# Optimization experiments

Hardware: AMD Instinct MI355X
Metric: run time of the kernel (lower is better)

The kernel has to match this reference:

```python
import jax, jax.numpy as jnp
import numpy as np

NITER = 3

def fft2c(x):
    x = jnp.fft.ifftshift(x, axes=(-2, -1))
    x = jnp.fft.fft2(x, axes=(-2, -1), norm='ortho')
    return jnp.fft.fftshift(x, axes=(-2, -1))

def ifft2c(x):
    x = jnp.fft.ifftshift(x, axes=(-2, -1))
    x = jnp.fft.ifft2(x, axes=(-2, -1), norm='ortho')
    return jnp.fft.fftshift(x, axes=(-2, -1))

def conv3d(x, w):
    # x: [N, D, H, W, C]; w: [3,3,3,Cin,Cout]; 'same' padding, stride 1, no bias
    return jax.lax.conv_general_dilated(x, w, window_strides=(1, 1, 1), padding='SAME',
                                        dimension_numbers=('NDHWC', 'DHWIO', 'NDHWC'))

def setup_inputs():
    key = jax.random.key(0)
    ks = jax.random.split(key, 16)
    nb, nt, nx, ny = 1, 18, 160, 160
    s = 0.05  # weight scale to keep unrolled iterations numerically tame
    d_real = jax.random.normal(ks[0], (nb, nt, nx, ny), jnp.float32)
    d_imag = jax.random.normal(ks[1], (nb, nt, nx, ny), jnp.float32)
    mask = jax.random.randint(ks[2], (nt, nx, ny), 0, 2, jnp.int32)
    W1 = jax.random.normal(ks[3], (NITER, 3, 3, 3, 2, 16), jnp.float32) * s
    W2 = jax.random.normal(ks[4], (NITER, 3, 3, 3, 16, 16), jnp.float32) * s
    W3 = jax.random.normal(ks[5], (NITER, 3, 3, 3, 16, 16), jnp.float32) * s
    W4 = jax.random.normal(ks[6], (NITER, 3, 3, 3, 16, 16), jnp.float32) * s
    W5 = jax.random.normal(ks[7], (NITER, 3, 3, 3, 16, 16), jnp.float32) * s
    W6 = jax.random.normal(ks[8], (NITER, 3, 3, 3, 16, 2), jnp.float32) * s
    lam1 = jnp.full((NITER,), 0.1, jnp.float32)       # lambda_step init
    lam2 = jnp.full((NITER,), 0.1, jnp.float32)       # lambda_step_2 init
    soft_thr = jnp.full((NITER,), 0.1, jnp.float32)
    thres_coef = jnp.full((NITER,), -2.0, jnp.float32)
    eta = jnp.full((NITER,), 0.01, jnp.float32)
    return dict(d_real=d_real, d_imag=d_imag, mask=mask, W1=W1, W2=W2, W3=W3, W4=W4,
                W5=W5, W6=W6, lam1=lam1, lam2=lam2, soft_thr=soft_thr,
                thres_coef=thres_coef, eta=eta)

def _slr_net(d_real, d_imag, mask, W1, W2, W3, W4, W5, W6, lam1, lam2, soft_thr, thres_coef, eta):
    d = jax.lax.complex(d_real, d_imag)          # [nb,nt,nx,ny] complex64
    m = mask.astype(jnp.complex64)               # [nt,nx,ny], broadcasts over batch
    x_rec = ifft2c(d * m)                        # E^H d
    t = jnp.zeros_like(x_rec)
    beta = jnp.zeros_like(x_rec)
    X_SYM = []
    for i in range(NITER):
        lam = jnp.maximum(lam1[i], 0.0).astype(jnp.complex64)
        lam2c = jnp.maximum(lam2[i], 0.0).astype(jnp.complex64)
        # data-consistency gradient: E^H (E x - d)
        ATAX = ifft2c(m * (m * fft2c(x_rec) - d))
        r_n = x_rec - lam * ATAX + lam2c * (x_rec + beta - t)
        r = jnp.stack([r_n.real, r_n.imag], axis=-1)  # [nb,nt,nx,ny,2]
        x1 = jax.nn.relu(conv3d(r, W1[i]))
        x2 = jax.nn.relu(conv3d(x1, W2[i]))
        x3 = conv3d(x2, W3[i])
        x_soft = jnp.sign(x3) * jax.nn.relu(jnp.abs(x3) - soft_thr[i])
        x4 = jax.nn.relu(conv3d(x_soft, W4[i]))
        x5 = jax.nn.relu(conv3d(x4, W5[i]))
        x6 = conv3d(x5, W6[i])
        x_out = x6 + r
        xs = jax.nn.relu(conv3d(x3, W4[i]))
        xs = jax.nn.relu(conv3d(xs, W5[i]))
        xs = conv3d(xs, W6[i])
        x_sym = xs - r
        x_rec = jax.lax.complex(x_out[..., 0], x_out[..., 1])
        # low-rank step: batched thin SVD with learned singular-value thresholding
        nb_, nt_, nx_, ny_ = x_rec.shape
        M = x_rec.reshape(nb_, nt_, nx_ * ny_)
        U, S, Vh = jnp.linalg.svd(M, full_matrices=False)   # U:[b,nt,nt] S:[b,nt] Vh:[b,nt,nx*ny]
        thres = jax.nn.sigmoid(thres_coef[i]) * S[:, :1]
        S = jax.nn.relu(S - thres)
        t = (U * S[:, None, :].astype(U.dtype)) @ Vh
        t = t.reshape(nb_, nt_, nx_, ny_)
        beta = beta + jnp.maximum(eta[i], 0.0).astype(jnp.complex64) * (x_rec - t)
        X_SYM.append(x_sym)
    return x_rec, jnp.stack(X_SYM)

def reference(d_real, d_imag, mask, W1, W2, W3, W4, W5, W6, lam1, lam2, soft_thr, thres_coef, eta):
    return _slr_net(d_real, d_imag, mask, W1, W2, W3, W4, W5, W6, lam1, lam2, soft_thr, thres_coef, eta)
```

## Files before the change

### kernel.cpp

```cpp
#include <hip/hip_runtime.h>
#include <hip/hip_fp16.h>

#define NT 18
#define NX 160
#define NY 160
#define NPIX (NX*NY)
#define NVOX (NT*NPIX)

typedef _Float16 __attribute__((ext_vector_type(2))) half2t;
typedef _Float16 __attribute__((ext_vector_type(8))) half8t;
typedef float    __attribute__((ext_vector_type(4))) f32x4;
typedef unsigned int u32;
typedef __attribute__((address_space(1))) const u32 gu32;
typedef __attribute__((address_space(3))) u32 lu32;

__global__ void probe_kernel(float* __restrict__ out, int n, float val) {
  int i = blockIdx.x * 256 + threadIdx.x;
  if (i < n) out[i] = val;
}

__global__ void make_g_kernel(float2* __restrict__ G) {
  int idx = blockIdx.x * 256 + threadIdx.x;
  if (idx >= NPIX) return;
  int r = idx / NY, c = idx - (idx / NY) * NY;
  int rs = (r + 80) % 160;
  int cs = (c + 80) % 160;
  int prod = (rs * cs) % 160;
  double ang = -2.0 * 3.14159265358979323846 * (double)prod / 160.0;
  double sc = 0.07905694150420949;
  G[idx] = make_float2((float)(cos(ang) * sc), (float)(sin(ang) * sc));
}

__global__ void zero_kernel(float* __restrict__ p, int n) {
  int i = blockIdx.x * 256 + threadIdx.x;
  if (i < n) p[i] = 0.f;
}

template <int MASKD>
__global__ void fft_pass_last4(const float2* __restrict__ in, float2* __restrict__ out,
                               const float2* __restrict__ G, int conjf,
                               const float* __restrict__ dr, const float* __restrict__ di,
                               const int* __restrict__ maskp) {
  __shared__ float2 rows[4][NY];
  int r0 = blockIdx.x * 4;
  int v = threadIdx.x;
#pragma unroll
  for (int r = 0; r < 4; ++r) {
    size_t idx = (size_t)(r0 + r) * NY + v;
    if (MASKD) {
      float m = (float)maskp[idx];
      rows[r][v] = make_float2(m * dr[idx], m * di[idx]);
    } else {
      rows[r][v] = in[idx];
    }
  }
  __syncthreads();
  float sgn = conjf ? -1.f : 1.f;
  float ar[4] = {0.f, 0.f, 0.f, 0.f}, ai[4] = {0.f, 0.f, 0.f, 0.f};
  for (int k = 0; k < NY; ++k) {
    float2 g = G[k * NY + v];
    float gi = sgn * g.y;
#pragma unroll
    for (int r = 0; r < 4; ++r) {
      float2 a = rows[r][k];
      ar[r] += a.x * g.x - a.y * gi;
      ai[r] += a.x * gi + a.y * g.x;
    }
  }
#pragma unroll
  for (int r = 0; r < 4; ++r)
    out[(size_t)(r0 + r) * NY + v] = make_float2(ar[r], ai[r]);
}

template <int EPI>
__global__ void fft_pass_mid4(const float2* __restrict__ in, void* __restrict__ outv,
                              const float2* __restrict__ G, int conjf,
                              const float* __restrict__ dr, const float* __restrict__ di,
                              const int* __restrict__ maskp,
                              const float2* __restrict__ xrec2, const float2* __restrict__ beta2,
                              const float2* __restrict__ tbuf2,
                              const float* __restrict__ l1p, const float* __restrict__ l2p) {
  __shared__ float2 grow[4][NX];
  int b = (int)blockIdx.x;
  int sb = (b & 7) * 90 + (b >> 3);
  int t = sb / 40;
  int u0 = (sb - t * 40) * 4;
  int v = threadIdx.x;
#pragma unroll
  for (int r = 0; r < 4; ++r) grow[r][v] = G[(u0 + r) * NX + v];
  __syncthreads();
  float sgn = conjf ? -1.f : 1.f;
  float ar[4] = {0.f, 0.f, 0.f, 0.f}, ai[4] = {0.f, 0.f, 0.f, 0.f};
  const float2* base = in + (size_t)t * NPIX;
  for (int j = 0; j < NX; ++j) {
    float2 a = base[j * NY + v];
#pragma unroll
    for (int r = 0; r < 4; ++r) {
      float2 g = grow[r][j];
      float gi = sgn * g.y;
      ar[r] += a.x * g.x - a.y * gi;
      ai[r] += a.x * gi + a.y * g.x;
    }
  }
  float l1 = 0.f, l2 = 0.f;
  if (EPI == 2) { l1 = fmaxf(l1p[0], 0.f); l2 = fmaxf(l2p[0], 0.f); }
#pragma unroll
  for (int r = 0; r < 4; ++r) {
    size_t idx = (size_t)t * NPIX + (size_t)(u0 + r) * NY + v;
    if (EPI == 0) {
      ((float2*)outv)[idx] = make_float2(ar[r], ai[r]);
    } else if (EPI == 1) {
      float m = (float)maskp[idx];
      ((float2*)outv)[idx] = make_float2(m * (m * ar[r] - dr[idx]),
                                         m * (m * ai[r] - di[idx]));
    } else {
      float2 x = xrec2[idx], bb = beta2[idx], tt = tbuf2[idx];
      ((float*)outv)[2 * idx]     = (1.f + l2) * x.x - l1 * ar[r] + l2 * (bb.x - tt.x);
      ((float*)outv)[2 * idx + 1] = (1.f + l2) * x.y - l1 * ai[r] + l2 * (bb.y - tt.y);
    }
  }
}

template <int MODE>
__device__ void eigen_part(const float2* __restrict__ Ain, float* __restrict__ scr,
                           const float* __restrict__ tcp, float2* __restrict__ Wout) {
  __shared__ float Ar[NT][NT], Ai_[NT][NT], Vr[NT][NT], Vi_[NT][NT];
  __shared__ float cS[9], sS[9], erS[9], eiS[9];
  __shared__ int pS[9], qS[9];
  __shared__ float ratio[NT];
  int tid = threadIdx.x;
  for (int idx = tid; idx < NT * NT; idx += 256) {
    int i = idx / NT, j = idx - (idx / NT) * NT;
    if (MODE == 1) {
      float2 a = Ain[idx];
      Ar[i][j] = a.x;
      Ai_[i][j] = (i == j) ? 0.f : a.y;
      Vr[i][j] = (i == j) ? 1.f : 0.f;
      Vi_[i][j] = 0.f;
    } else {
      Ar[i][j] = scr[idx];
      Ai_[i][j] = scr[324 + idx];
      Vr[i][j] = scr[648 + idx];
      Vi_[i][j] = scr[972 + idx];
    }
  }
  __syncthreads();
  for (int sweep = 0; sweep < 2; ++sweep) {
    for (int r = 0; r < NT - 1; ++r) {
      if (tid < 9) {
        int k = tid;
        int a = (r + k) % (NT - 1);
        int b = (k == 0) ? (NT - 1) : (r - k + (NT - 1)) % (NT - 1);
        int p = min(a, b), q = max(a, b);
        pS[k] = p; qS[k] = q;
        float apr = Ar[p][q], api = Ai_[p][q];
        float r2 = apr * apr + api * api;
        float c = 1.f, s = 0.f, er = 1.f, ei = 0.f;
        if (r2 > 1e-28f) {
          float rr = sqrtf(r2);
          float inv_r = 1.f / rr;
          er = apr * inv_r; ei = api * inv_r;
          float th = (Ar[q][q] - Ar[p][p]) * 0.5f * inv_r;
          float tt = (th >= 0.f ? 1.f : -1.f) / (fabsf(th) + sqrtf(th * th + 1.f));
          c = 1.f / sqrtf(tt * tt + 1.f);
          s = tt * c;
        }
        cS[k] = c; sS[k] = s; erS[k] = er; eiS[k] = ei;
      }
      __syncthreads();
      if (tid < 9 * NT) {
        int idx = tid;
        int k = idx / 9, j = idx - (idx / 9) * 9;
        int p = pS[j], q = qS[j];
        float c = cS[j], s = sS[j], er = erS[j], ei = eiS[j];
        float apr = Ar[k][p], api = Ai_[k][p];
        float aqr = Ar[k][q], aqi = Ai_[k][q];
        float eqr = er * aqr + ei * aqi;
        float eqi = er * aqi - ei * aqr;
        Ar[k][p] = c * apr - s * eqr;  Ai_[k][p] = c * api - s * eqi;
        Ar[k][q] = s * apr + c * eqr;  Ai_[k][q] = s * api + c * eqi;
        float vpr = Vr[k][p], vpi = Vi_[k][p];
        float vqr = Vr[k][q], vqi = Vi_[k][q];
        float evr = er * vqr + ei * vqi;
        float evi = er * vqi - ei * vqr;
        Vr[k][p] = c * vpr - s * evr;  Vi_[k][p] = c * vpi - s * evi;
        Vr[k][q] = s * vpr + c * evr;  Vi_[k][q] = s * vpi + c * evi;
      }
      __syncthreads();
      if (tid < 9 * NT) {
        int idx = tid;
        int k = idx / 9, j = idx - (idx / 9) * 9;
        int p = pS[j], q = qS[j];
        float c = cS[j], s = sS[j], er = erS[j], ei = eiS[j];
        float bpr = Ar[p][k], bpi = Ai_[p][k];
        float bqr = Ar[q][k], bqi = Ai_[q][k];
        float ebr = er * bqr - ei * bqi;
        float ebi = er * bqi + ei * bqr;
        Ar[p][k] = c * bpr - s * ebr;  Ai_[p][k] = c * bpi - s * ebi;
        Ar[q][k] = s * bpr + c * ebr;  Ai_[q][k] = s * bpi + c * ebi;
      }
      __syncthreads();
    }
  }
  if (MODE == 3) {
    if (tid == 0) {
      float smax = 0.f;
      for (int k = 0; k < NT; ++k) {
        float sv = sqrtf(fmaxf(Ar[k][k], 0.f));
        ratio[k] = sv;
        smax = fmaxf(smax, sv);
      }
      float sig = 1.f / (1.f + expf(-tcp[0]));
      float thres = sig * smax;
      for (int k = 0; k < NT; ++k) {
        float sv = ratio[k];
        ratio[k] = (sv > thres) ? (sv - thres) / sv : 0.f;
      }
    }
    __syncthreads();
    for (int idx = tid; idx < NT * NT; idx += 256) {
      int i = idx / NT, j = idx - (idx / NT) * NT;
      float wr = 0.f, wi = 0.f;
      for (int k = 0; k < NT; ++k) {
        float rk = ratio[k];
        wr += rk * (Vr[i][k] * Vr[j][k] + Vi_[i][k] * Vi_[j][k]);
        wi += rk * (Vi_[i][k] * Vr[j][k] - Vr[i][k] * Vi_[j][k]);
      }
      Wout[idx] = make_float2(wr, wi);
    }
  } else {
    for (int idx = tid; idx < NT * NT; idx += 256) {
      int i = idx / NT, j = idx - (idx / NT) * NT;
      scr[idx]       = Ar[i][j];
      scr[324 + idx] = Ai_[i][j];
      scr[648 + idx] = Vr[i][j];
      scr[972 + idx] = Vi_[i][j];
    }
  }
}

#define ROWCH 164
#define NROWS 18
#define NCHUNK (NROWS*ROWCH)
#define NBLK 1440

template <int COUT, bool RELU, int OUTMODE, bool SOFT, int EIG, bool PAIRED>
__global__ void __launch_bounds__(256)
conv3d_mfma_kernel(const __half* __restrict__ in_, const float* __restrict__ wts,
                   void* __restrict__ out_, const float* __restrict__ res, float resSign,
                   const float* __restrict__ thrp,
                   const float2* __restrict__ eigA, float* __restrict__ eigScr,
                   const float* __restrict__ tcp, float2* __restrict__ eigW,
                   float* __restrict__ outReal,
                   const __half* __restrict__ in1, void* __restrict__ out1, float resSign1) {
  if constexpr (EIG > 0) {
    if (blockIdx.x == 0) { eigen_part<EIG>(eigA, eigScr, tcp, eigW); return; }
  }
  __shared__ alignas(16) __half lds[NCHUNK * 8];
  const int tid = threadIdx.x;
  int bid0 = (EIG > 0) ? ((int)blockIdx.x - 1) : (int)blockIdx.x;
  const __half* inp = in_;
  void* outp = out_;
  float rs = resSign;
  bool dosoft = SOFT;
  float* oreal = outReal;
  if (PAIRED && bid0 >= NBLK) {
    bid0 -= NBLK; inp = in1; outp = out1; rs = resSign1; dosoft = false; oreal = nullptr;
  }
  const int bid = (bid0 & 7) * 180 + (bid0 >> 3);
  const int z   = bid / 80;
  const int rem = bid - z * 80;
  const int y0  = (rem >> 1) * 4;
  const int xbase = (rem & 1) * 80;

  const int lane = tid & 63;
  const int wv = tid >> 6;
  const int n = lane & 15;
  const int g = lane >> 4;
  const int sel = g >> 1;
  const int ci = (g & 1) * 8;

  half8t bw[14];
#pragma unroll
  for (int c = 0; c < 14; ++c) {
#pragma unroll
    for (int j = 0; j < 8; ++j) {
      int kg = c * 32 + g * 8 + j;
      float w = (kg < 432 && n < COUT) ? wts[kg * COUT + n] : 0.f;
      bw[c][j] = (_Float16)w;
    }
  }

  if (!dosoft) {
    half8t zero8 = {0, 0, 0, 0, 0, 0, 0, 0};
    if (tid < 2 * NROWS) {
      int row = tid >> 1, which = tid & 1;
      int off = (xbase == 0) ? which : (162 + which);
      *reinterpret_cast<half8t*>(&lds[(row * ROWCH + off) * 8]) = zero8;
    }
#pragma unroll 1
    for (int row = 0; row < NROWS; ++row) {
      int zz = z - 1 + row / 6;
      int yy = y0 - 1 + row % 6;
      if ((unsigned)zz >= (unsigned)NT || (unsigned)yy >= (unsigned)NX) {
        for (int i = tid; i < ROWCH; i += 256)
          *reinterpret_cast<half8t*>(&lds[(row * ROWCH + i) * 8]) = zero8;
      }
    }
    const int wb = tid & ~63;
#pragma unroll 1
    for (int base = 0; base < NCHUNK; base += 256) {
      int i = base + tid;
      if (i < NCHUNK) {
        int row = i / ROWCH;
        int off = i - row * ROWCH;
        int zz = z - 1 + row / 6;
        int yy = y0 - 1 + row % 6;
        int x = xbase - 1 + (off >> 1);
        bool valid = ((unsigned)zz < (unsigned)NT) && ((unsigned)yy < (unsigned)NX) &&
                     ((unsigned)x < (unsigned)NY);
        if (valid) {
          const __half* src = inp + ((size_t)((zz * NX + yy) * NY + x)) * 16 + (off & 1) * 8;
          __builtin_amdgcn_global_load_lds(
              (gu32*)(const void*)src,
              (lu32*)(void*)&lds[(size_t)(base + wb) * 8],
              16, 0, 0);
        }
      }
    }
  } else {
    float thr = SOFT ? thrp[0] : 0.f;
    for (int i = tid; i < NCHUNK; i += 256) {
      int row = i / ROWCH;
      int off = i - row * ROWCH;
      int zz = z - 1 + row / 6;
      int yy = y0 - 1 + row % 6;
      int x = xbase - 1 + (off >> 1);
      half8t v = {0, 0, 0, 0, 0, 0, 0, 0};
      if ((unsigned)zz < (unsigned)NT && (unsigned)yy < (unsigned)NX &&
          (unsigned)x < (unsigned)NY) {
        v = *reinterpret_cast<const half8t*>(
              inp + ((size_t)((zz * NX + yy) * NY + x)) * 16 + (off & 1) * 8);
#pragma unroll
        for (int e = 0; e < 8; ++e) {
          float f = (float)v[e];
          v[e] = (_Float16)copysignf(fmaxf(fabsf(f) - thr, 0.f), f);
        }
      }
      *reinterpret_cast<half8t*>(&lds[(size_t)i * 8]) = v;
    }
  }
  __syncthreads();

  const int yloc = wv;
#pragma unroll 1
  for (int t = 0; t < 5; ++t) {
    int xloc = t * 16;

    f32x4 acc = {0.f, 0.f, 0.f, 0.f};
#pragma unroll
    for (int c = 0; c < 14; ++c) {
      const int t0 = 2 * c, t1 = 2 * c + 1;
      const int dz0 = t0 / 9, dy0 = (t0 / 3) % 3, dx0 = t0 % 3;
      const int dz1 = t1 / 9, dy1 = (t1 / 3) % 3, dx1 = t1 % 3;
      half8t a = {0, 0, 0, 0, 0, 0, 0, 0};
      if (c < 13 || !sel) {
        int dz = sel ? dz1 : dz0;
        int dy = sel ? dy1 : dy0;
        int dx = sel ? dx1 : dx0;
        int rowi = dz * 6 + yloc + dy;
        int slot = xloc + n + dx;
        int aoff = rowi * (ROWCH * 8) + slot * 16 + ci;
        a = *reinterpret_cast<const half8t*>(&lds[aoff]);
      }
      acc = __builtin_amdgcn_mfma_f32_16x16x32_f16(a, bw[c], acc, 0, 0, 0);
    }

    size_t vb = ((size_t)(z * NX) + (y0 + yloc)) * NY + xbase + xloc;
    if (n < COUT) {
#pragma unroll
      for (int r = 0; r < 4; ++r) {
        float v = acc[r];
        size_t oidx = (vb + g * 4 + r) * COUT + n;
        if (res) v += rs * res[oidx];
        if (RELU) v = fmaxf(v, 0.f);
        if (OUTMODE == 1) ((__half*)outp)[oidx] = __float2half(v);
        else {
          ((float*)outp)[oidx] = v;
          if (COUT == 2 && oreal && n == 0) oreal[vb + g * 4 + r] = v;
        }
      }
    }
  }
}

template <bool RELU>
__global__ void __launch_bounds__(256)
conv3d_mfma2in_kernel(const float* __restrict__ in_, const float* __restrict__ wts,
                      __half* __restrict__ out_) {
  __shared__ alignas(8) __half lds2[12 * 324];
  const int tid = threadIdx.x;
  const int bid0 = (int)blockIdx.x;
  const int bid = (bid0 & 7) * 180 + (bid0 >> 3);
  const int z  = bid / 80;
  const int y0 = (bid - z * 80) * 2;
  const int lane = tid & 63;
  const int wv = tid >> 6;
  const int n = lane & 15;
  const int g = lane >> 4;

  half8t bw[2];
#pragma unroll
  for (int c = 0; c < 2; ++c) {
#pragma unroll
    for (int j = 0; j < 8; ++j) {
      int k = c * 32 + g * 8 + j;
      float w = (k < 54) ? wts[k * 16 + n] : 0.f;
      bw[c][j] = (_Float16)w;
    }
  }

  for (int i = tid; i < 12 * 162; i += 256) {
    int row = i / 162;
    int vox = i - row * 162;
    int zz = z - 1 + (row >> 2);
    int yy = y0 - 1 + (row & 3);
    int xx = vox - 1;
    half2t v2 = {(_Float16)0.f, (_Float16)0.f};
    if ((unsigned)zz < (unsigned)NT && (unsigned)yy < (unsigned)NX && (unsigned)xx < (unsigned)NY) {
      float2 f = reinterpret_cast<const float2*>(in_)[(size_t)(zz * NX + yy) * NY + xx];
      v2[0] = (_Float16)f.x;
      v2[1] = (_Float16)f.y;
    }
    *reinterpret_cast<half2t*>(&lds2[i * 2]) = v2;
  }
  __syncthreads();

#pragma unroll 1
  for (int t = 0; t < 5; ++t) {
    int tl = wv * 5 + t;
    int yloc = (tl >= 10) ? 1 : 0;
    int x0 = (tl - yloc * 10) * 16;
    f32x4 acc = {0.f, 0.f, 0.f, 0.f};
#pragma unroll
    for (int c = 0; c < 2; ++c) {
      half8t a = {0, 0, 0, 0, 0, 0, 0, 0};
#pragma unroll
      for (int u = 0; u < 4; ++u) {
        int tap = c * 16 + g * 4 + u;
        if (tap < 27) {
          int dz = tap / 9, dy = (tap / 3) % 3, dx = tap % 3;
          int rowi = dz * 4 + yloc + dy;
          half2t p = *reinterpret_cast<const half2t*>(&lds2[rowi * 324 + (x0 + n + dx) * 2]);
          a[2 * u] = p[0];
          a[2 * u + 1] = p[1];
        }
      }
      acc = __builtin_amdgcn_mfma_f32_16x16x32_f16(a, bw[c], acc, 0, 0, 0);
    }
    size_t vb = ((size_t)(z * NX) + (y0 + yloc)) * NY + x0;
#pragma unroll
    for (int r = 0; r < 4; ++r) {
      float v = acc[r];
      if (RELU) v = fmaxf(v, 0.f);
      out_[(vb + g * 4 + r) * 16 + n] = __float2half(v);
    }
  }
}

__global__ void gram_kernel(const float2* __restrict__ M, float2* __restrict__ A) {
  int b = blockIdx.x;
  int i = 0;
  while (b >= NT - i) { b -= NT - i; ++i; }
  int j = i + b;
  int tid = threadIdx.x;
  float sr = 0.f, si = 0.f;
  for (int p = tid; p < NPIX; p += 256) {
    float2 a = M[(size_t)i * NPIX + p];
    float2 c = M[(size_t)j * NPIX + p];
    sr += a.x * c.x + a.y * c.y;
    si += a.y * c.x - a.x * c.y;
  }
  __shared__ float rs[256], is_[256];
  rs[tid] = sr; is_[tid] = si;
  __syncthreads();
  for (int s = 128; s > 0; s >>= 1) {
    if (tid < s) { rs[tid] += rs[tid + s]; is_[tid] += is_[tid + s]; }
    __syncthreads();
  }
  if (tid == 0) {
    A[i * NT + j] = make_float2(rs[0], is_[0]);
    if (i != j) A[j * NT + i] = make_float2(rs[0], -is_[0]);
  }
}

__global__ void svd_apply_kernel(const float2* __restrict__ M, const float2* __restrict__ Wm,
                                 float2* __restrict__ t, float2* __restrict__ beta,
                                 const float* __restrict__ etap) {
  __shared__ float2 W[NT * NT];
  int tid = threadIdx.x;
  for (int i = tid; i < NT * NT; i += 256) W[i] = Wm[i];
  __syncthreads();
  int p = blockIdx.x * 256 + tid;
  float eta = fmaxf(etap[0], 0.f);
  float2 m[NT];
#pragma unroll
  for (int j = 0; j < NT; ++j) m[j] = M[(size_t)j * NPIX + p];
#pragma unroll
  for (int i = 0; i < NT; ++i) {
    float tr = 0.f, ti = 0.f;
#pragma unroll
    for (int j = 0; j < NT; ++j) {
      float2 w = W[i * NT + j];
      tr += w.x * m[j].x - w.y * m[j].y;
      ti += w.x * m[j].y + w.y * m[j].x;
    }
    t[(size_t)i * NPIX + p] = make_float2(tr, ti);
    float2 b = beta[(size_t)i * NPIX + p];
    b.x += eta * (m[i].x - tr);
    b.y += eta * (m[i].y - ti);
    beta[(size_t)i * NPIX + p] = b;
  }
}

extern "C" void kernel_launch(void* const* d_in, const int* in_sizes, int n_in,
                              void* d_out, int out_size, void* d_ws, size_t ws_size,
                              hipStream_t stream) {
  const float* d_real    = (const float*)d_in[0];
  const float* d_imag    = (const float*)d_in[1];
  const int*   mask      = (const int*)d_in[2];
  const float* W1        = (const float*)d_in[3];
  const float* W2        = (const float*)d_in[4];
  const float* W3        = (const float*)d_in[5];
  const float* W4        = (const float*)d_in[6];
  const float* W5        = (const float*)d_in[7];
  const float* W6        = (const float*)d_in[8];
  const float* lam1      = (const float*)d_in[9];
  const float* lam2      = (const float*)d_in[10];
  const float* soft_thr  = (const float*)d_in[11];
  const float* thres_c   = (const float*)d_in[12];
  const float* eta       = (const float*)d_in[13];
  float* out = (float*)d_out;
  (void)in_sizes; (void)n_in;

  const size_t NEEDED = 74200000ull;
  if (ws_size < NEEDED) {
    probe_kernel<<<(out_size + 255) / 256, 256, 0, stream>>>(out, out_size,
                                                             (float)(ws_size >> 20));
    return;
  }

  char* wp_ = (char*)d_ws;
  auto alloc = [&](size_t bytes) {
    char* r = wp_;
    wp_ += (bytes + 255) & ~(size_t)255;
    return r;
  };
  float2* G      = (float2*)alloc((size_t)NPIX * sizeof(float2));
  float2* xrec   = (float2*)alloc((size_t)NVOX * sizeof(float2));
  float2* tbuf   = (float2*)alloc((size_t)NVOX * sizeof(float2));
  float2* beta   = (float2*)alloc((size_t)NVOX * sizeof(float2));
  float*  Rf     = (float*)alloc((size_t)NVOX * 2 * sizeof(float));
  __half* Af     = (__half*)alloc((size_t)NVOX * 16 * sizeof(__half));
  __half* Bf     = (__half*)alloc((size_t)NVOX * 16 * sizeof(__half));
  __half* Cf     = (__half*)alloc((size_t)NVOX * 16 * sizeof(__half));
  __half* Df     = (__half*)alloc((size_t)NVOX * 16 * sizeof(__half));
  float2* Agram  = (float2*)alloc((size_t)NT * NT * sizeof(float2));
  float2* Wmat   = (float2*)alloc((size_t)NT * NT * sizeof(float2));
  float*  EigScr = (float*)alloc(1296 * sizeof(float));
  float2* T1 = (float2*)Af;
  float2* T2 = (float2*)Bf;

  make_g_kernel<<<100, 256, 0, stream>>>(G);
  zero_kernel<<<7200, 256, 0, stream>>>((float*)tbuf, 4 * NVOX);

  fft_pass_last4<1><<<720, 160, 0, stream>>>(nullptr, T2, G, 1, d_real, d_imag, mask);
  fft_pass_mid4<0><<<720, 160, 0, stream>>>(T2, xrec, G, 1, nullptr, nullptr, nullptr,
                                            nullptr, nullptr, nullptr, nullptr, nullptr);

  for (int i = 0; i < 3; ++i) {
    fft_pass_last4<0><<<720, 160, 0, stream>>>(xrec, T1, G, 0, nullptr, nullptr, nullptr);
    fft_pass_mid4<1><<<720, 160, 0, stream>>>(T1, T2, G, 0, d_real, d_imag, mask,
                                              nullptr, nullptr, nullptr, nullptr, nullptr);
    fft_pass_last4<0><<<720, 160, 0, stream>>>(T2, T1, G, 1, nullptr, nullptr, nullptr);
    fft_pass_mid4<2><<<720, 160, 0, stream>>>(T1, Rf, G, 1, nullptr, nullptr, nullptr,
                                              xrec, beta, tbuf, lam1 + i, lam2 + i);
    conv3d_mfma2in_kernel<true><<<1440, 256, 0, stream>>>(Rf, W1 + (size_t)i * 864, Af);
    conv3d_mfma_kernel<16, true, 1, false, 0, false><<<1440, 256, 0, stream>>>(
        Af, W2 + (size_t)i * 6912, Bf, nullptr, 0.f, nullptr,
        nullptr, nullptr, nullptr, nullptr, nullptr, nullptr, nullptr, 0.f);
    conv3d_mfma_kernel<16, false, 1, false, 0, false><<<1440, 256, 0, stream>>>(
        Bf, W3 + (size_t)i * 6912, Cf, nullptr, 0.f, nullptr,
        nullptr, nullptr, nullptr, nullptr, nullptr, nullptr, nullptr, 0.f);

    if (i < 2) {
      conv3d_mfma_kernel<16, true, 1, true, 0, false><<<1440, 256, 0, stream>>>(
          Cf, W4 + (size_t)i * 6912, Bf, nullptr, 0.f, soft_thr + i,
          nullptr, nullptr, nullptr, nullptr, nullptr, nullptr, nullptr, 0.f);
      conv3d_mfma_kernel<16, true, 1, false, 0, false><<<1440, 256, 0, stream>>>(
          Bf, W5 + (size_t)i * 6912, Af, nullptr, 0.f, nullptr,
          nullptr, nullptr, nullptr, nullptr, nullptr, nullptr, nullptr, 0.f);
      conv3d_mfma_kernel<2, false, 0, false, 0, false><<<1440, 256, 0, stream>>>(
          Af, W6 + (size_t)i * 864, (float*)xrec, Rf, 1.f, nullptr,
          nullptr, nullptr, nullptr, nullptr, nullptr, nullptr, nullptr, 0.f);
      gram_kernel<<<171, 256, 0, stream>>>((const float2*)xrec, Agram);
      conv3d_mfma_kernel<16, true, 1, false, 1, false><<<1441, 256, 0, stream>>>(
          Cf, W4 + (size_t)i * 6912, Bf, nullptr, 0.f, nullptr,
          Agram, EigScr, thres_c + i, Wmat, nullptr, nullptr, nullptr, 0.f);
      conv3d_mfma_kernel<16, true, 1, false, 2, false><<<1441, 256, 0, stream>>>(
          Bf, W5 + (size_t)i * 6912, Af, nullptr, 0.f, nullptr,
          Agram, EigScr, thres_c + i, Wmat, nullptr, nullptr, nullptr, 0.f);
      conv3d_mfma_kernel<2, false, 0, false, 3, false><<<1441, 256, 0, stream>>>(
          Af, W6 + (size_t)i * 864, out + 460800 + (size_t)921600 * i, Rf, -1.f, nullptr,
          Agram, EigScr, thres_c + i, Wmat, nullptr, nullptr, nullptr, 0.f);
      svd_apply_kernel<<<100, 256, 0, stream>>>((const float2*)xrec, Wmat, tbuf, beta, eta + i);
    } else {
      conv3d_mfma_kernel<16, true, 1, true, 0, true><<<2880, 256, 0, stream>>>(
          Cf, W4 + (size_t)i * 6912, Bf, nullptr, 0.f, soft_thr + i,
          nullptr, nullptr, nullptr, nullptr, nullptr, Cf, Df, 0.f);
      conv3d_mfma_kernel<16, true, 1, false, 0, true><<<2880, 256, 0, stream>>>(
          Bf, W5 + (size_t)i * 6912, Af, nullptr, 0.f, nullptr,
          nullptr, nullptr, nullptr, nullptr, nullptr, Df, Cf, 0.f);
      conv3d_mfma_kernel<2, false, 0, false, 0, true><<<2880, 256, 0, stream>>>(
          Af, W6 + (size_t)i * 864, (float*)xrec, Rf, 1.f, nullptr,
          nullptr, nullptr, nullptr, nullptr, out,
          Cf, out + 460800 + (size_t)921600 * i, -1.f);
    }
  }
}
```

Baseline: 1.199 ms.

## Double DFT rows per block and skip zero-init of beta/t buffers on first iteration

The DFT-by-matrix passes now compute 8 rows per block instead of 4, which halves the grid and reuses each loaded G or input element across more accumulators. The first iteration uses new specialized epilogues that assume beta and t are zero, so the zero-fill kernel and the reads of beta/tbuf on iteration 0 go away. The svd_apply kernel gets a FIRST variant that writes beta directly instead of read-modify-write. Fewer blocks (360) may underfill the GPU, and more accumulators raise register pressure.

```diff
diff --git a/kernel.cpp b/kernel.cpp
--- a/kernel.cpp
+++ b/kernel.cpp
@@ -31,21 +31,18 @@
   G[idx] = make_float2((float)(cos(ang) * sc), (float)(sin(ang) * sc));
 }
 
-__global__ void zero_kernel(float* __restrict__ p, int n) {
-  int i = blockIdx.x * 256 + threadIdx.x;
-  if (i < n) p[i] = 0.f;
-}
-
 template <int MASKD>
-__global__ void fft_pass_last4(const float2* __restrict__ in, float2* __restrict__ out,
+__global__ void fft_pass_last8(const float2* __restrict__ in, float2* __restrict__ out,
                                const float2* __restrict__ G, int conjf,
                                const float* __restrict__ dr, const float* __restrict__ di,
                                const int* __restrict__ maskp) {
-  __shared__ float2 rows[4][NY];
-  int r0 = blockIdx.x * 4;
+  __shared__ float2 rows[8][NY];
+  int b = (int)blockIdx.x;
+  int sb = (b & 7) * 45 + (b >> 3);
+  int r0 = sb * 8;
   int v = threadIdx.x;
 #pragma unroll
-  for (int r = 0; r < 4; ++r) {
+  for (int r = 0; r < 8; ++r) {
     size_t idx = (size_t)(r0 + r) * NY + v;
     if (MASKD) {
       float m = (float)maskp[idx];
@@ -56,46 +53,48 @@
   }
   __syncthreads();
   float sgn = conjf ? -1.f : 1.f;
-  float ar[4] = {0.f, 0.f, 0.f, 0.f}, ai[4] = {0.f, 0.f, 0.f, 0.f};
+  float ar[8] = {0.f, 0.f, 0.f, 0.f, 0.f, 0.f, 0.f, 0.f};
+  float ai[8] = {0.f, 0.f, 0.f, 0.f, 0.f, 0.f, 0.f, 0.f};
   for (int k = 0; k < NY; ++k) {
     float2 g = G[k * NY + v];
     float gi = sgn * g.y;
 #pragma unroll
-    for (int r = 0; r < 4; ++r) {
+    for (int r = 0; r < 8; ++r) {
       float2 a = rows[r][k];
       ar[r] += a.x * g.x - a.y * gi;
       ai[r] += a.x * gi + a.y * g.x;
     }
   }
 #pragma unroll
-  for (int r = 0; r < 4; ++r)
+  for (int r = 0; r < 8; ++r)
     out[(size_t)(r0 + r) * NY + v] = make_float2(ar[r], ai[r]);
 }
 
 template <int EPI>
-__global__ void fft_pass_mid4(const float2* __restrict__ in, void* __restrict__ outv,
+__global__ void fft_pass_mid8(const float2* __restrict__ in, void* __restrict__ outv,
                               const float2* __restrict__ G, int conjf,
                               const float* __restrict__ dr, const float* __restrict__ di,
                               const int* __restrict__ maskp,
                               const float2* __restrict__ xrec2, const float2* __restrict__ beta2,
                               const float2* __restrict__ tbuf2,
                               const float* __restrict__ l1p, const float* __restrict__ l2p) {
-  __shared__ float2 grow[4][NX];
+  __shared__ float2 grow[8][NX];
   int b = (int)blockIdx.x;
-  int sb = (b & 7) * 90 + (b >> 3);
-  int t = sb / 40;
-  int u0 = (sb - t * 40) * 4;
+  int sb = (b & 7) * 45 + (b >> 3);
+  int t = sb / 20;
+  int u0 = (sb - t * 20) * 8;
   int v = threadIdx.x;
 #pragma unroll
-  for (int r = 0; r < 4; ++r) grow[r][v] = G[(u0 + r) * NX + v];
+  for (int r = 0; r < 8; ++r) grow[r][v] = G[(u0 + r) * NX + v];
   __syncthreads();
   float sgn = conjf ? -1.f : 1.f;
-  float ar[4] = {0.f, 0.f, 0.f, 0.f}, ai[4] = {0.f, 0.f, 0.f, 0.f};
+  float ar[8] = {0.f, 0.f, 0.f, 0.f, 0.f, 0.f, 0.f, 0.f};
+  float ai[8] = {0.f, 0.f, 0.f, 0.f, 0.f, 0.f, 0.f, 0.f};
   const float2* base = in + (size_t)t * NPIX;
   for (int j = 0; j < NX; ++j) {
     float2 a = base[j * NY + v];
 #pragma unroll
-    for (int r = 0; r < 4; ++r) {
+    for (int r = 0; r < 8; ++r) {
       float2 g = grow[r][j];
       float gi = sgn * g.y;
       ar[r] += a.x * g.x - a.y * gi;
@@ -103,9 +102,9 @@
     }
   }
   float l1 = 0.f, l2 = 0.f;
-  if (EPI == 2) { l1 = fmaxf(l1p[0], 0.f); l2 = fmaxf(l2p[0], 0.f); }
-#pragma unroll
-  for (int r = 0; r < 4; ++r) {
+  if (EPI >= 2) { l1 = fmaxf(l1p[0], 0.f); l2 = fmaxf(l2p[0], 0.f); }
+#pragma unroll
+  for (int r = 0; r < 8; ++r) {
     size_t idx = (size_t)t * NPIX + (size_t)(u0 + r) * NY + v;
     if (EPI == 0) {
       ((float2*)outv)[idx] = make_float2(ar[r], ai[r]);
@@ -113,10 +112,14 @@
       float m = (float)maskp[idx];
       ((float2*)outv)[idx] = make_float2(m * (m * ar[r] - dr[idx]),
                                          m * (m * ai[r] - di[idx]));
-    } else {
+    } else if (EPI == 2) {
       float2 x = xrec2[idx], bb = beta2[idx], tt = tbuf2[idx];
       ((float*)outv)[2 * idx]     = (1.f + l2) * x.x - l1 * ar[r] + l2 * (bb.x - tt.x);
       ((float*)outv)[2 * idx + 1] = (1.f + l2) * x.y - l1 * ai[r] + l2 * (bb.y - tt.y);
+    } else {
+      float2 x = xrec2[idx];
+      ((float*)outv)[2 * idx]     = (1.f + l2) * x.x - l1 * ar[r];
+      ((float*)outv)[2 * idx + 1] = (1.f + l2) * x.y - l1 * ai[r];
     }
   }
 }
@@ -494,6 +497,7 @@
   }
 }
 
+template <bool FIRST>
 __global__ void svd_apply_kernel(const float2* __restrict__ M, const float2* __restrict__ Wm,
                                  float2* __restrict__ t, float2* __restrict__ beta,
                                  const float* __restrict__ etap) {
@@ -516,10 +520,14 @@
       ti += w.x * m[j].y + w.y * m[j].x;
     }
     t[(size_t)i * NPIX + p] = make_float2(tr, ti);
-    float2 b = beta[(size_t)i * NPIX + p];
-    b.x += eta * (m[i].x - tr);
-    b.y += eta * (m[i].y - ti);
-    beta[(size_t)i * NPIX + p] = b;
+    if (FIRST) {
+      beta[(size_t)i * NPIX + p] = make_float2(eta * (m[i].x - tr), eta * (m[i].y - ti));
+    } else {
+      float2 b = beta[(size_t)i * NPIX + p];
+      b.x += eta * (m[i].x - tr);
+      b.y += eta * (m[i].y - ti);
+      beta[(size_t)i * NPIX + p] = b;
+    }
   }
 }
 
@@ -572,19 +580,23 @@
   float2* T2 = (float2*)Bf;
 
   make_g_kernel<<<100, 256, 0, stream>>>(G);
-  zero_kernel<<<7200, 256, 0, stream>>>((float*)tbuf, 4 * NVOX);
-
-  fft_pass_last4<1><<<720, 160, 0, stream>>>(nullptr, T2, G, 1, d_real, d_imag, mask);
-  fft_pass_mid4<0><<<720, 160, 0, stream>>>(T2, xrec, G, 1, nullptr, nullptr, nullptr,
+
+  fft_pass_last8<1><<<360, 160, 0, stream>>>(nullptr, T2, G, 1, d_real, d_imag, mask);
+  fft_pass_mid8<0><<<360, 160, 0, stream>>>(T2, xrec, G, 1, nullptr, nullptr, nullptr,
                                             nullptr, nullptr, nullptr, nullptr, nullptr);
 
   for (int i = 0; i < 3; ++i) {
-    fft_pass_last4<0><<<720, 160, 0, stream>>>(xrec, T1, G, 0, nullptr, nullptr, nullptr);
-    fft_pass_mid4<1><<<720, 160, 0, stream>>>(T1, T2, G, 0, d_real, d_imag, mask,
+    fft_pass_last8<0><<<360, 160, 0, stream>>>(xrec, T1, G, 0, nullptr, nullptr, nullptr);
+    fft_pass_mid8<1><<<360, 160, 0, stream>>>(T1, T2, G, 0, d_real, d_imag, mask,
                                               nullptr, nullptr, nullptr, nullptr, nullptr);
-    fft_pass_last4<0><<<720, 160, 0, stream>>>(T2, T1, G, 1, nullptr, nullptr, nullptr);
-    fft_pass_mid4<2><<<720, 160, 0, stream>>>(T1, Rf, G, 1, nullptr, nullptr, nullptr,
-                                              xrec, beta, tbuf, lam1 + i, lam2 + i);
+    fft_pass_last8<0><<<360, 160, 0, stream>>>(T2, T1, G, 1, nullptr, nullptr, nullptr);
+    if (i == 0) {
+      fft_pass_mid8<3><<<360, 160, 0, stream>>>(T1, Rf, G, 1, nullptr, nullptr, nullptr,
+                                                xrec, nullptr, nullptr, lam1 + i, lam2 + i);
+    } else {
+      fft_pass_mid8<2><<<360, 160, 0, stream>>>(T1, Rf, G, 1, nullptr, nullptr, nullptr,
+                                                xrec, beta, tbuf, lam1 + i, lam2 + i);
+    }
     conv3d_mfma2in_kernel<true><<<1440, 256, 0, stream>>>(Rf, W1 + (size_t)i * 864, Af);
     conv3d_mfma_kernel<16, true, 1, false, 0, false><<<1440, 256, 0, stream>>>(
         Af, W2 + (size_t)i * 6912, Bf, nullptr, 0.f, nullptr,
@@ -613,7 +625,10 @@
       conv3d_mfma_kernel<2, false, 0, false, 3, false><<<1441, 256, 0, stream>>>(
           Af, W6 + (size_t)i * 864, out + 460800 + (size_t)921600 * i, Rf, -1.f, nullptr,
           Agram, EigScr, thres_c + i, Wmat, nullptr, nullptr, nullptr, 0.f);
-      svd_apply_kernel<<<100, 256, 0, stream>>>((const float2*)xrec, Wmat, tbuf, beta, eta + i);
+      if (i == 0)
+        svd_apply_kernel<true><<<100, 256, 0, stream>>>((const float2*)xrec, Wmat, tbuf, beta, eta + i);
+      else
+        svd_apply_kernel<false><<<100, 256, 0, stream>>>((const float2*)xrec, Wmat, tbuf, beta, eta + i);
     } else {
       conv3d_mfma_kernel<16, true, 1, true, 0, true><<<2880, 256, 0, stream>>>(
           Cf, W4 + (size_t)i * 6912, Bf, nullptr, 0.f, soft_thr + i,
```

New measurement: 1.359 ms. +13.3%, slower.
